# Kernel optimization log

Hardware: AMD Instinct MI355X
Metric: run time of the kernel (lower is better)

## Reference

```python
import jax, jax.numpy as jnp
import numpy as np

N_NODES = 100000


def sage_conv(x, src, dst, w_self, w_neigh, b):
    # DGL SAGEConv('mean'): h = x @ W_self + mean_{u in N(v)} x_u @ W_neigh + b
    ones = jnp.ones(src.shape[0], dtype=x.dtype)
    deg = jax.ops.segment_sum(ones, dst, num_segments=N_NODES)  # [N]
    neigh_sum = jax.ops.segment_sum(x[src], dst, num_segments=N_NODES)  # [N, F]
    neigh = neigh_sum / jnp.clip(deg, 1.0)[:, None]  # isolated nodes -> 0
    return x @ w_self + neigh @ w_neigh + b


def setup_inputs() -> dict:
    key = jax.random.key(0)
    ks = jax.random.split(key, 9)
    nfeat, nhid, nclass = 128, 128, 2
    E = 1600000
    x = jax.random.normal(ks[0], (N_NODES, nfeat), dtype=jnp.float32)
    src = jax.random.randint(ks[1], (E,), 0, N_NODES)
    dst = jax.random.randint(ks[2], (E,), 0, N_NODES)
    s1 = 1.0 / np.sqrt(nfeat)
    s2 = 1.0 / np.sqrt(nhid)
    return {
        "x": x,
        "src": src,
        "dst": dst,
        "w_self1": jax.random.uniform(ks[3], (nfeat, nhid), jnp.float32, -s1, s1),
        "w_neigh1": jax.random.uniform(ks[4], (nfeat, nhid), jnp.float32, -s1, s1),
        "b1": jnp.zeros((nhid,), jnp.float32),
        "w_self2": jax.random.uniform(ks[5], (nhid, nclass), jnp.float32, -s2, s2),
        "w_neigh2": jax.random.uniform(ks[6], (nhid, nclass), jnp.float32, -s2, s2),
        "b2": jnp.zeros((nclass,), jnp.float32),
    }


def reference(x, src, dst, w_self1, w_neigh1, b1, w_self2, w_neigh2, b2):
    h = jax.nn.relu(sage_conv(x, src, dst, w_self1, w_neigh1, b1))
    h = sage_conv(h, src, dst, w_self2, w_neigh2, b2)
    return jax.nn.log_softmax(h, axis=1)
```

## Files before the change

kernel.cpp:

```cpp
#include <hip/hip_runtime.h>
#include <hip/hip_bf16.h>


#define N_FEAT 128
#define CSHIFT 10
#define CNODES 1024
#define CCAP 18432
#define BATCH 4096

typedef __attribute__((ext_vector_type(8))) short short8;
typedef __attribute__((ext_vector_type(8))) unsigned short ushort8_t;
typedef __attribute__((ext_vector_type(16))) float f32x16;

__global__ __launch_bounds__(256) void multisplit_kernel(
    const int* __restrict__ src, const int* __restrict__ dst,
    int* __restrict__ ccursor, unsigned* __restrict__ cbuf, int E) {
    __shared__ unsigned stage[BATCH];
    __shared__ int cnt[128];
    __shared__ int s[128];
    __shared__ int excl[128];
    __shared__ int incl[128];
    __shared__ int cur[128];
    __shared__ int gpos[128];
    int tid = threadIdx.x;
    int base = blockIdx.x * BATCH;
    int total = min(BATCH, E - base);

    unsigned pk[16];
    int bn[16];
    if (tid < 128) cnt[tid] = 0;
    __syncthreads();
    #pragma unroll
    for (int k = 0; k < 16; ++k) {
        int e = base + k * 256 + tid;
        if (e < E) {
            int d = dst[e];
            int sv = src[e];
            bn[k] = d >> CSHIFT;
            pk[k] = ((unsigned)(d & (CNODES - 1)) << 17) | (unsigned)sv;
            atomicAdd(&cnt[bn[k]], 1);
        } else {
            bn[k] = -1;
        }
    }
    __syncthreads();
    int c = (tid < 128) ? cnt[tid] : 0;
    int val = c;
    if (tid < 128) s[tid] = val;
    __syncthreads();
    for (int off = 1; off < 128; off <<= 1) {
        int t = (tid >= off && tid < 128) ? s[tid - off] : 0;
        __syncthreads();
        if (tid < 128) { val += t; s[tid] = val; }
        __syncthreads();
    }
    if (tid < 128) {
        incl[tid] = val;
        excl[tid] = val - c;
        cur[tid] = val - c;
        gpos[tid] = (c > 0) ? atomicAdd(&ccursor[tid], c) : 0;
    }
    __syncthreads();
    #pragma unroll
    for (int k = 0; k < 16; ++k) {
        if (bn[k] >= 0) {
            int ofs = atomicAdd(&cur[bn[k]], 1);
            stage[ofs] = pk[k];
        }
    }
    __syncthreads();
    for (int i = tid; i < total; i += 256) {
        int lo = 0, hi = 127;
        while (lo < hi) {
            int mid = (lo + hi) >> 1;
            if (incl[mid] > i) hi = mid; else lo = mid + 1;
        }
        int b = lo;
        int target = gpos[b] + (i - excl[b]);
        cbuf[(size_t)b * CCAP + target] = stage[i];
    }
}

__global__ void coarse_scan_kernel(const int* __restrict__ ccnt, int* __restrict__ cstart,
                                   int* __restrict__ row_ptr, int nbk, int N, int E) {
    __shared__ int s[128];
    int tid = threadIdx.x;
    int c = (tid < nbk) ? ccnt[tid] : 0;
    int val = c;
    s[tid] = val;
    __syncthreads();
    for (int off = 1; off < 128; off <<= 1) {
        int t = (tid >= off) ? s[tid - off] : 0;
        __syncthreads();
        val += t;
        s[tid] = val;
        __syncthreads();
    }
    if (tid < nbk) cstart[tid] = val - c;
    if (tid == 0) row_ptr[N] = E;
}

__global__ __launch_bounds__(1024) void build_csr2_kernel(
    const unsigned* __restrict__ cbuf, const int* __restrict__ ccnt,
    const int* __restrict__ cstart, int* __restrict__ row_ptr,
    int* __restrict__ csr, int N) {
    __shared__ int hist[CNODES];
    __shared__ int s[CNODES];
    __shared__ int cur[CNODES];
    int cb = blockIdx.x;
    int tid = threadIdx.x;
    int cnt = ccnt[cb];
    int base = cstart[cb];
    size_t bbase = (size_t)cb * CCAP;
    hist[tid] = 0;
    __syncthreads();
    for (int e = tid; e < cnt; e += 1024) {
        unsigned p = cbuf[bbase + e];
        atomicAdd(&hist[p >> 17], 1);
    }
    __syncthreads();
    int c = hist[tid];
    int val = c;
    s[tid] = val;
    __syncthreads();
    for (int off = 1; off < 1024; off <<= 1) {
        int t = (tid >= off) ? s[tid - off] : 0;
        __syncthreads();
        val += t;
        s[tid] = val;
        __syncthreads();
    }
    int excl = val - c;
    int node = cb * CNODES + tid;
    if (node < N) row_ptr[node] = base + excl;
    cur[tid] = excl;
    __syncthreads();
    for (int e = tid; e < cnt; e += 1024) {
        unsigned p = cbuf[bbase + e];
        int bin = p >> 17;
        int ofs = atomicAdd(&cur[bin], 1);
        csr[base + ofs] = (int)(p & 0x1FFFF);
    }
}

__global__ void to_bf16_kernel(const float* __restrict__ x, ushort* __restrict__ xb, int n4) {
    int i = blockIdx.x * 256 + threadIdx.x;
    int stride = gridDim.x * 256;
    for (; i < n4; i += stride) {
        float4 v = ((const float4*)x)[i];
        ushort4 r;
        r.x = __bfloat16_as_ushort(__float2bfloat16(v.x));
        r.y = __bfloat16_as_ushort(__float2bfloat16(v.y));
        r.z = __bfloat16_as_ushort(__float2bfloat16(v.z));
        r.w = __bfloat16_as_ushort(__float2bfloat16(v.w));
        ((ushort4*)xb)[i] = r;
    }
}

__global__ void prep_weights_kernel(const float* __restrict__ w1, const float* __restrict__ w2,
                                    ushort* __restrict__ wt) {
    int id = blockIdx.x * 256 + threadIdx.x;
    if (id >= 128 * 256) return;
    int nn = id >> 8;
    int k = id & 255;
    float v = (k < 128) ? w1[k * 128 + nn] : w2[(k - 128) * 128 + nn];
    wt[nn * 256 + k] = __bfloat16_as_ushort(__float2bfloat16(v));
}

__device__ __forceinline__ float bf16_bits_to_f32(ushort u) {
    union { unsigned int i; float f; } c;
    c.i = ((unsigned int)u) << 16;
    return c.f;
}

__global__ void aggregate_bf16_kernel(const ushort* __restrict__ xb,
                                      const int* __restrict__ row_ptr,
                                      const int* __restrict__ csr,
                                      ushort* __restrict__ out, int n) {
    int v = blockIdx.x * 4 + (threadIdx.x >> 6);
    int lane = threadIdx.x & 63;
    if (v >= n) return;
    int beg = row_ptr[v];
    int end = row_ptr[v + 1];
    float a0 = 0.f, b0 = 0.f, a1 = 0.f, b1 = 0.f;
    int e = beg;
    for (; e + 4 <= end; e += 4) {
        int s0 = csr[e], s1 = csr[e + 1], s2 = csr[e + 2], s3 = csr[e + 3];
        ushort2 t0 = ((const ushort2*)(xb + (size_t)s0 * N_FEAT))[lane];
        ushort2 t1 = ((const ushort2*)(xb + (size_t)s1 * N_FEAT))[lane];
        ushort2 t2 = ((const ushort2*)(xb + (size_t)s2 * N_FEAT))[lane];
        ushort2 t3 = ((const ushort2*)(xb + (size_t)s3 * N_FEAT))[lane];
        a0 += bf16_bits_to_f32(t0.x); b0 += bf16_bits_to_f32(t0.y);
        a1 += bf16_bits_to_f32(t1.x); b1 += bf16_bits_to_f32(t1.y);
        a0 += bf16_bits_to_f32(t2.x); b0 += bf16_bits_to_f32(t2.y);
        a1 += bf16_bits_to_f32(t3.x); b1 += bf16_bits_to_f32(t3.y);
    }
    for (; e < end; ++e) {
        int s0 = csr[e];
        ushort2 t0 = ((const ushort2*)(xb + (size_t)s0 * N_FEAT))[lane];
        a0 += bf16_bits_to_f32(t0.x); b0 += bf16_bits_to_f32(t0.y);
    }
    int deg = end - beg;
    float inv = (deg > 0) ? 1.0f / (float)deg : 0.0f;
    ushort2 r;
    r.x = __bfloat16_as_ushort(__float2bfloat16((a0 + a1) * inv));
    r.y = __bfloat16_as_ushort(__float2bfloat16((b0 + b1) * inv));
    ((ushort2*)(out + (size_t)v * N_FEAT))[lane] = r;
}

__global__ __launch_bounds__(256) void gemm1_mfma_kernel(
    const ushort* __restrict__ xb, const ushort* __restrict__ nbb,
    const ushort* __restrict__ wt, const float* __restrict__ b,
    ushort* __restrict__ h, int n) {
    __shared__ ushort As[128 * 72];
    __shared__ ushort Bs[128 * 72];
    int tid = threadIdx.x;
    int wave = tid >> 6;
    int lane = tid & 63;
    int m = lane & 31;
    int half = lane >> 5;
    int block_row = blockIdx.x * 128;

    f32x16 acc[4];
    #pragma unroll
    for (int t = 0; t < 4; ++t)
        #pragma unroll
        for (int i = 0; i < 16; ++i) acc[t][i] = 0.0f;

    for (int kc = 0; kc < 4; ++kc) {
        const ushort* A = (kc < 2) ? xb : nbb;
        int k0 = (kc & 1) * 64;
        #pragma unroll
        for (int l = 0; l < 4; ++l) {
            int idx = l * 256 + tid;
            int r = idx >> 3;
            int p = idx & 7;
            int node = block_row + r;
            ushort8_t v;
            if (node < n) {
                v = *(const ushort8_t*)(A + (size_t)node * N_FEAT + k0 + p * 8);
            } else {
                #pragma unroll
                for (int q = 0; q < 8; ++q) v[q] = 0;
            }
            *(ushort8_t*)(&As[r * 72 + p * 8]) = v;
        }
        #pragma unroll
        for (int l = 0; l < 4; ++l) {
            int idx = l * 256 + tid;
            int cc = idx >> 3;
            int p = idx & 7;
            ushort8_t v = *(const ushort8_t*)(wt + (size_t)cc * 256 + kc * 64 + p * 8);
            *(ushort8_t*)(&Bs[cc * 72 + p * 8]) = v;
        }
        __syncthreads();
        #pragma unroll
        for (int ks = 0; ks < 4; ++ks) {
            int koff = ks * 16 + half * 8;
            short8 a = *(const short8*)(&As[(32 * wave + m) * 72 + koff]);
            short8 bf0 = *(const short8*)(&Bs[(0 * 32 + m) * 72 + koff]);
            short8 bf1 = *(const short8*)(&Bs[(1 * 32 + m) * 72 + koff]);
            short8 bf2 = *(const short8*)(&Bs[(2 * 32 + m) * 72 + koff]);
            short8 bf3 = *(const short8*)(&Bs[(3 * 32 + m) * 72 + koff]);
            acc[0] = __builtin_amdgcn_mfma_f32_32x32x16_bf16(a, bf0, acc[0], 0, 0, 0);
            acc[1] = __builtin_amdgcn_mfma_f32_32x32x16_bf16(a, bf1, acc[1], 0, 0, 0);
            acc[2] = __builtin_amdgcn_mfma_f32_32x32x16_bf16(a, bf2, acc[2], 0, 0, 0);
            acc[3] = __builtin_amdgcn_mfma_f32_32x32x16_bf16(a, bf3, acc[3], 0, 0, 0);
        }
        __syncthreads();
    }
    #pragma unroll
    for (int t = 0; t < 4; ++t) {
        int col = t * 32 + m;
        float bias = b[col];
        #pragma unroll
        for (int reg = 0; reg < 16; ++reg) {
            int rowin = (reg & 3) + 8 * (reg >> 2) + 4 * half;
            int node = block_row + 32 * wave + rowin;
            if (node < n) {
                float v = fmaxf(acc[t][reg] + bias, 0.0f);
                h[(size_t)node * N_FEAT + col] = __bfloat16_as_ushort(__float2bfloat16(v));
            }
        }
    }
}

__global__ void layer2a_kernel(const ushort* __restrict__ h,
                               const float* __restrict__ ws, const float* __restrict__ wn,
                               float* __restrict__ s_out, float* __restrict__ z_out, int n) {
    int v = blockIdx.x * 4 + (threadIdx.x >> 6);
    int lane = threadIdx.x & 63;
    if (v >= n) return;
    ushort2 hb = ((const ushort2*)(h + (size_t)v * N_FEAT))[lane];
    float hx = bf16_bits_to_f32(hb.x);
    float hy = bf16_bits_to_f32(hb.y);
    float4 w0 = ((const float4*)ws)[lane];
    float4 w1 = ((const float4*)wn)[lane];
    float p0 = hx * w0.x + hy * w0.z;
    float p1 = hx * w0.y + hy * w0.w;
    float q0 = hx * w1.x + hy * w1.z;
    float q1 = hx * w1.y + hy * w1.w;
    #pragma unroll
    for (int off = 32; off > 0; off >>= 1) {
        p0 += __shfl_xor(p0, off);
        p1 += __shfl_xor(p1, off);
        q0 += __shfl_xor(q0, off);
        q1 += __shfl_xor(q1, off);
    }
    if (lane == 0) {
        ((float2*)s_out)[v] = make_float2(p0, p1);
        ((float2*)z_out)[v] = make_float2(q0, q1);
    }
}

__global__ void layer2b_kernel(const float* __restrict__ s_in, const float* __restrict__ z,
                               const int* __restrict__ row_ptr, const int* __restrict__ csr,
                               const float* __restrict__ b, float* __restrict__ out, int n) {
    int v = blockIdx.x * 256 + threadIdx.x;
    if (v >= n) return;
    int beg = row_ptr[v];
    int end = row_ptr[v + 1];
    float a0 = 0.f, a1 = 0.f, c0 = 0.f, c1 = 0.f;
    int e = beg;
    for (; e + 2 <= end; e += 2) {
        float2 t0 = ((const float2*)z)[csr[e]];
        float2 t1 = ((const float2*)z)[csr[e + 1]];
        a0 += t0.x; a1 += t0.y;
        c0 += t1.x; c1 += t1.y;
    }
    if (e < end) {
        float2 t0 = ((const float2*)z)[csr[e]];
        a0 += t0.x; a1 += t0.y;
    }
    int deg = end - beg;
    float inv = (deg > 0) ? 1.0f / (float)deg : 0.0f;
    float2 sv = ((const float2*)s_in)[v];
    float o0 = sv.x + (a0 + c0) * inv + b[0];
    float o1 = sv.y + (a1 + c1) * inv + b[1];
    float mx = fmaxf(o0, o1);
    float lse = mx + logf(expf(o0 - mx) + expf(o1 - mx));
    ((float2*)out)[v] = make_float2(o0 - lse, o1 - lse);
}

extern "C" void kernel_launch(void* const* d_in, const int* in_sizes, int n_in,
                              void* d_out, int out_size, void* d_ws, size_t ws_size,
                              hipStream_t stream) {
    const float* x        = (const float*)d_in[0];
    const int*   src      = (const int*)d_in[1];
    const int*   dst      = (const int*)d_in[2];
    const float* w_self1  = (const float*)d_in[3];
    const float* w_neigh1 = (const float*)d_in[4];
    const float* b1       = (const float*)d_in[5];
    const float* w_self2  = (const float*)d_in[6];
    const float* w_neigh2 = (const float*)d_in[7];
    const float* b2       = (const float*)d_in[8];
    float* out = (float*)d_out;

    int N = in_sizes[0] / N_FEAT;
    int E = in_sizes[1];
    int nbk = (N + CNODES - 1) / CNODES;

    char* ws = (char*)d_ws;
    size_t off = 0;
    auto alloc = [&](size_t bytes) -> void* {
        void* p = ws + off;
        off += (bytes + 255) & ~(size_t)255;
        return p;
    };
    int*      ccursor = (int*)alloc(128 * 4);
    int*      cstart  = (int*)alloc(128 * 4);
    int*      row_ptr = (int*)alloc((size_t)(N + 1) * 4);
    int*      csr     = (int*)alloc((size_t)E * 4);
    unsigned* cbuf    = (unsigned*)alloc((size_t)nbk * CCAP * 4);
    ushort*   xb      = (ushort*)alloc((size_t)N * N_FEAT * 2);
    ushort*   nbb     = (ushort*)alloc((size_t)N * N_FEAT * 2);
    ushort*   h       = (ushort*)alloc((size_t)N * N_FEAT * 2);
    ushort*   wt      = (ushort*)alloc((size_t)128 * 256 * 2);
    float*    s_buf   = (float*)alloc((size_t)N * 2 * 4);
    float*    z_buf   = (float*)alloc((size_t)N * 2 * 4);
    (void)ws_size; (void)n_in; (void)out_size;

    hipMemsetAsync(ccursor, 0, 128 * 4, stream);

    multisplit_kernel<<<(E + BATCH - 1) / BATCH, 256, 0, stream>>>(src, dst, ccursor, cbuf, E);
    coarse_scan_kernel<<<1, 128, 0, stream>>>(ccursor, cstart, row_ptr, nbk, N, E);
    build_csr2_kernel<<<nbk, 1024, 0, stream>>>(cbuf, ccursor, cstart, row_ptr, csr, N);

    to_bf16_kernel<<<1024, 256, 0, stream>>>(x, xb, N * N_FEAT / 4);
    prep_weights_kernel<<<(128 * 256 + 255) / 256, 256, 0, stream>>>(w_self1, w_neigh1, wt);
    aggregate_bf16_kernel<<<(N + 3) / 4, 256, 0, stream>>>(xb, row_ptr, csr, nbb, N);
    gemm1_mfma_kernel<<<(N + 127) / 128, 256, 0, stream>>>(xb, nbb, wt, b1, h, N);
    layer2a_kernel<<<(N + 3) / 4, 256, 0, stream>>>(h, w_self2, w_neigh2, s_buf, z_buf, N);
    layer2b_kernel<<<(N + 255) / 256, 256, 0, stream>>>(s_buf, z_buf, row_ptr, csr, b2, out, N);
}
```

Baseline: 284.2 us.

## Fuse preprocessing kernels, inline coarse scan, fuse layer-2 projection into GEMM epilogue

Merges the edge multisplit, bf16 conversion of x and weight packing into one launch with role-split blocks. The coarse scan moves into each build_csr2 block, and multisplit uses per-wave counters to cut LDS atomic contention. The aggregation loop is unrolled to 8 edges, and the layer-2 projection is fused into the GEMM1 epilogue, which removes the h buffer round trip and two launches. Costs are redundant scans per block and extra shuffle reductions in the GEMM epilogue.

```diff
diff --git a/kernel.cpp b/kernel.cpp
--- a/kernel.cpp
+++ b/kernel.cpp
@@ -7,28 +7,60 @@
 #define CNODES 1024
 #define CCAP 18432
 #define BATCH 4096
+#define BF_BLOCKS 256
+#define PW_BLOCKS 128
 
 typedef __attribute__((ext_vector_type(8))) short short8;
 typedef __attribute__((ext_vector_type(8))) unsigned short ushort8_t;
 typedef __attribute__((ext_vector_type(16))) float f32x16;
 
-__global__ __launch_bounds__(256) void multisplit_kernel(
+__global__ __launch_bounds__(256) void prep_and_split_kernel(
     const int* __restrict__ src, const int* __restrict__ dst,
-    int* __restrict__ ccursor, unsigned* __restrict__ cbuf, int E) {
+    int* __restrict__ ccursor, unsigned* __restrict__ cbuf, int E,
+    const float* __restrict__ x, ushort* __restrict__ xb, int n4,
+    const float* __restrict__ w1, const float* __restrict__ w2,
+    ushort* __restrict__ wt, int nms) {
     __shared__ unsigned stage[BATCH];
-    __shared__ int cnt[128];
+    __shared__ int cntw[4][128];
+    __shared__ int curw[4][128];
     __shared__ int s[128];
     __shared__ int excl[128];
     __shared__ int incl[128];
-    __shared__ int cur[128];
     __shared__ int gpos[128];
     int tid = threadIdx.x;
-    int base = blockIdx.x * BATCH;
+    int bid = blockIdx.x;
+
+    if (bid >= nms) {
+        int rb = bid - nms;
+        if (rb < BF_BLOCKS) {
+            int i = rb * 256 + tid;
+            int stride = BF_BLOCKS * 256;
+            for (; i < n4; i += stride) {
+                float4 v = ((const float4*)x)[i];
+                ushort4 r;
+                r.x = __bfloat16_as_ushort(__float2bfloat16(v.x));
+                r.y = __bfloat16_as_ushort(__float2bfloat16(v.y));
+                r.z = __bfloat16_as_ushort(__float2bfloat16(v.z));
+                r.w = __bfloat16_as_ushort(__float2bfloat16(v.w));
+                ((ushort4*)xb)[i] = r;
+            }
+        } else {
+            int id = (rb - BF_BLOCKS) * 256 + tid;
+            int nn = id >> 8;
+            int k = id & 255;
+            float v = (k < 128) ? w1[k * 128 + nn] : w2[(k - 128) * 128 + nn];
+            wt[nn * 256 + k] = __bfloat16_as_ushort(__float2bfloat16(v));
+        }
+        return;
+    }
+
+    int wv = tid >> 6;
+    int base = bid * BATCH;
     int total = min(BATCH, E - base);
 
     unsigned pk[16];
     int bn[16];
-    if (tid < 128) cnt[tid] = 0;
+    for (int i = tid; i < 512; i += 256) ((int*)cntw)[i] = 0;
     __syncthreads();
     #pragma unroll
     for (int k = 0; k < 16; ++k) {
@@ -38,16 +70,24 @@
             int sv = src[e];
             bn[k] = d >> CSHIFT;
             pk[k] = ((unsigned)(d & (CNODES - 1)) << 17) | (unsigned)sv;
-            atomicAdd(&cnt[bn[k]], 1);
+            atomicAdd(&cntw[wv][bn[k]], 1);
         } else {
             bn[k] = -1;
         }
     }
     __syncthreads();
-    int c = (tid < 128) ? cnt[tid] : 0;
+    int c = 0;
+    if (tid < 128) {
+        int c0 = cntw[0][tid], c1 = cntw[1][tid], c2 = cntw[2][tid], c3 = cntw[3][tid];
+        cntw[0][tid] = 0;
+        cntw[1][tid] = c0;
+        cntw[2][tid] = c0 + c1;
+        cntw[3][tid] = c0 + c1 + c2;
+        c = c0 + c1 + c2 + c3;
+        s[tid] = c;
+    }
+    __syncthreads();
     int val = c;
-    if (tid < 128) s[tid] = val;
-    __syncthreads();
     for (int off = 1; off < 128; off <<= 1) {
         int t = (tid >= off && tid < 128) ? s[tid - off] : 0;
         __syncthreads();
@@ -56,15 +96,19 @@
     }
     if (tid < 128) {
         incl[tid] = val;
-        excl[tid] = val - c;
-        cur[tid] = val - c;
+        int e0 = val - c;
+        excl[tid] = e0;
+        curw[0][tid] = e0 + cntw[0][tid];
+        curw[1][tid] = e0 + cntw[1][tid];
+        curw[2][tid] = e0 + cntw[2][tid];
+        curw[3][tid] = e0 + cntw[3][tid];
         gpos[tid] = (c > 0) ? atomicAdd(&ccursor[tid], c) : 0;
     }
     __syncthreads();
     #pragma unroll
     for (int k = 0; k < 16; ++k) {
         if (bn[k] >= 0) {
-            int ofs = atomicAdd(&cur[bn[k]], 1);
+            int ofs = atomicAdd(&curw[wv][bn[k]], 1);
             stage[ofs] = pk[k];
         }
     }
@@ -81,37 +125,33 @@
     }
 }
 
-__global__ void coarse_scan_kernel(const int* __restrict__ ccnt, int* __restrict__ cstart,
-                                   int* __restrict__ row_ptr, int nbk, int N, int E) {
-    __shared__ int s[128];
-    int tid = threadIdx.x;
-    int c = (tid < nbk) ? ccnt[tid] : 0;
-    int val = c;
-    s[tid] = val;
-    __syncthreads();
-    for (int off = 1; off < 128; off <<= 1) {
-        int t = (tid >= off) ? s[tid - off] : 0;
-        __syncthreads();
-        val += t;
-        s[tid] = val;
-        __syncthreads();
-    }
-    if (tid < nbk) cstart[tid] = val - c;
-    if (tid == 0) row_ptr[N] = E;
-}
-
 __global__ __launch_bounds__(1024) void build_csr2_kernel(
     const unsigned* __restrict__ cbuf, const int* __restrict__ ccnt,
-    const int* __restrict__ cstart, int* __restrict__ row_ptr,
-    int* __restrict__ csr, int N) {
+    int* __restrict__ row_ptr, int* __restrict__ csr, int N, int E) {
     __shared__ int hist[CNODES];
     __shared__ int s[CNODES];
     __shared__ int cur[CNODES];
+    __shared__ int cstart_s;
     int cb = blockIdx.x;
     int tid = threadIdx.x;
+
+    int c0 = 0;
+    if (tid < 128) { c0 = ccnt[tid]; s[tid] = c0; }
+    __syncthreads();
+    int v128 = c0;
+    for (int off = 1; off < 128; off <<= 1) {
+        int t = (tid >= off && tid < 128) ? s[tid - off] : 0;
+        __syncthreads();
+        if (tid < 128) { v128 += t; s[tid] = v128; }
+        __syncthreads();
+    }
+    if (tid == cb) cstart_s = v128 - c0;
+    if (cb == 0 && tid == 0) row_ptr[N] = E;
+    __syncthreads();
     int cnt = ccnt[cb];
-    int base = cstart[cb];
+    int base = cstart_s;
     size_t bbase = (size_t)cb * CCAP;
+
     hist[tid] = 0;
     __syncthreads();
     for (int e = tid; e < cnt; e += 1024) {
@@ -141,30 +181,6 @@
         int ofs = atomicAdd(&cur[bin], 1);
         csr[base + ofs] = (int)(p & 0x1FFFF);
     }
-}
-
-__global__ void to_bf16_kernel(const float* __restrict__ x, ushort* __restrict__ xb, int n4) {
-    int i = blockIdx.x * 256 + threadIdx.x;
-    int stride = gridDim.x * 256;
-    for (; i < n4; i += stride) {
-        float4 v = ((const float4*)x)[i];
-        ushort4 r;
-        r.x = __bfloat16_as_ushort(__float2bfloat16(v.x));
-        r.y = __bfloat16_as_ushort(__float2bfloat16(v.y));
-        r.z = __bfloat16_as_ushort(__float2bfloat16(v.z));
-        r.w = __bfloat16_as_ushort(__float2bfloat16(v.w));
-        ((ushort4*)xb)[i] = r;
-    }
-}
-
-__global__ void prep_weights_kernel(const float* __restrict__ w1, const float* __restrict__ w2,
-                                    ushort* __restrict__ wt) {
-    int id = blockIdx.x * 256 + threadIdx.x;
-    if (id >= 128 * 256) return;
-    int nn = id >> 8;
-    int k = id & 255;
-    float v = (k < 128) ? w1[k * 128 + nn] : w2[(k - 128) * 128 + nn];
-    wt[nn * 256 + k] = __bfloat16_as_ushort(__float2bfloat16(v));
 }
 
 __device__ __forceinline__ float bf16_bits_to_f32(ushort u) {
@@ -184,6 +200,26 @@
     int end = row_ptr[v + 1];
     float a0 = 0.f, b0 = 0.f, a1 = 0.f, b1 = 0.f;
     int e = beg;
+    for (; e + 8 <= end; e += 8) {
+        int s0 = csr[e],     s1 = csr[e + 1], s2 = csr[e + 2], s3 = csr[e + 3];
+        int s4 = csr[e + 4], s5 = csr[e + 5], s6 = csr[e + 6], s7 = csr[e + 7];
+        ushort2 t0 = ((const ushort2*)(xb + (size_t)s0 * N_FEAT))[lane];
+        ushort2 t1 = ((const ushort2*)(xb + (size_t)s1 * N_FEAT))[lane];
+        ushort2 t2 = ((const ushort2*)(xb + (size_t)s2 * N_FEAT))[lane];
+        ushort2 t3 = ((const ushort2*)(xb + (size_t)s3 * N_FEAT))[lane];
+        ushort2 t4 = ((const ushort2*)(xb + (size_t)s4 * N_FEAT))[lane];
+        ushort2 t5 = ((const ushort2*)(xb + (size_t)s5 * N_FEAT))[lane];
+        ushort2 t6 = ((const ushort2*)(xb + (size_t)s6 * N_FEAT))[lane];
+        ushort2 t7 = ((const ushort2*)(xb + (size_t)s7 * N_FEAT))[lane];
+        a0 += bf16_bits_to_f32(t0.x); b0 += bf16_bits_to_f32(t0.y);
+        a1 += bf16_bits_to_f32(t1.x); b1 += bf16_bits_to_f32(t1.y);
+        a0 += bf16_bits_to_f32(t2.x); b0 += bf16_bits_to_f32(t2.y);
+        a1 += bf16_bits_to_f32(t3.x); b1 += bf16_bits_to_f32(t3.y);
+        a0 += bf16_bits_to_f32(t4.x); b0 += bf16_bits_to_f32(t4.y);
+        a1 += bf16_bits_to_f32(t5.x); b1 += bf16_bits_to_f32(t5.y);
+        a0 += bf16_bits_to_f32(t6.x); b0 += bf16_bits_to_f32(t6.y);
+        a1 += bf16_bits_to_f32(t7.x); b1 += bf16_bits_to_f32(t7.y);
+    }
     for (; e + 4 <= end; e += 4) {
         int s0 = csr[e], s1 = csr[e + 1], s2 = csr[e + 2], s3 = csr[e + 3];
         ushort2 t0 = ((const ushort2*)(xb + (size_t)s0 * N_FEAT))[lane];
@@ -208,10 +244,11 @@
     ((ushort2*)(out + (size_t)v * N_FEAT))[lane] = r;
 }
 
-__global__ __launch_bounds__(256) void gemm1_mfma_kernel(
+__global__ __launch_bounds__(256) void gemm1_fused_kernel(
     const ushort* __restrict__ xb, const ushort* __restrict__ nbb,
     const ushort* __restrict__ wt, const float* __restrict__ b,
-    ushort* __restrict__ h, int n) {
+    const float* __restrict__ ws2, const float* __restrict__ wn2,
+    float* __restrict__ s_out, float* __restrict__ z_out, int n) {
     __shared__ ushort As[128 * 72];
     __shared__ ushort Bs[128 * 72];
     int tid = threadIdx.x;
@@ -269,47 +306,39 @@
         }
         __syncthreads();
     }
+
+    float bcol[4], wsc[4][2], wnc[4][2];
     #pragma unroll
     for (int t = 0; t < 4; ++t) {
         int col = t * 32 + m;
-        float bias = b[col];
-        #pragma unroll
-        for (int reg = 0; reg < 16; ++reg) {
-            int rowin = (reg & 3) + 8 * (reg >> 2) + 4 * half;
-            int node = block_row + 32 * wave + rowin;
-            if (node < n) {
-                float v = fmaxf(acc[t][reg] + bias, 0.0f);
-                h[(size_t)node * N_FEAT + col] = __bfloat16_as_ushort(__float2bfloat16(v));
-            }
-        }
-    }
-}
-
-__global__ void layer2a_kernel(const ushort* __restrict__ h,
-                               const float* __restrict__ ws, const float* __restrict__ wn,
-                               float* __restrict__ s_out, float* __restrict__ z_out, int n) {
-    int v = blockIdx.x * 4 + (threadIdx.x >> 6);
-    int lane = threadIdx.x & 63;
-    if (v >= n) return;
-    ushort2 hb = ((const ushort2*)(h + (size_t)v * N_FEAT))[lane];
-    float hx = bf16_bits_to_f32(hb.x);
-    float hy = bf16_bits_to_f32(hb.y);
-    float4 w0 = ((const float4*)ws)[lane];
-    float4 w1 = ((const float4*)wn)[lane];
-    float p0 = hx * w0.x + hy * w0.z;
-    float p1 = hx * w0.y + hy * w0.w;
-    float q0 = hx * w1.x + hy * w1.z;
-    float q1 = hx * w1.y + hy * w1.w;
+        bcol[t] = b[col];
+        float2 a = ((const float2*)ws2)[col];
+        float2 q = ((const float2*)wn2)[col];
+        wsc[t][0] = a.x; wsc[t][1] = a.y;
+        wnc[t][0] = q.x; wnc[t][1] = q.y;
+    }
     #pragma unroll
-    for (int off = 32; off > 0; off >>= 1) {
-        p0 += __shfl_xor(p0, off);
-        p1 += __shfl_xor(p1, off);
-        q0 += __shfl_xor(q0, off);
-        q1 += __shfl_xor(q1, off);
-    }
-    if (lane == 0) {
-        ((float2*)s_out)[v] = make_float2(p0, p1);
-        ((float2*)z_out)[v] = make_float2(q0, q1);
+    for (int reg = 0; reg < 16; ++reg) {
+        int rowin = (reg & 3) + 8 * (reg >> 2) + 4 * half;
+        int node = block_row + 32 * wave + rowin;
+        float p0 = 0.f, p1 = 0.f, q0 = 0.f, q1 = 0.f;
+        #pragma unroll
+        for (int t = 0; t < 4; ++t) {
+            float hv = fmaxf(acc[t][reg] + bcol[t], 0.0f);
+            p0 += hv * wsc[t][0]; p1 += hv * wsc[t][1];
+            q0 += hv * wnc[t][0]; q1 += hv * wnc[t][1];
+        }
+        #pragma unroll
+        for (int off = 1; off < 32; off <<= 1) {
+            p0 += __shfl_xor(p0, off);
+            p1 += __shfl_xor(p1, off);
+            q0 += __shfl_xor(q0, off);
+            q1 += __shfl_xor(q1, off);
+        }
+        if (m == 0 && node < n) {
+            ((float2*)s_out)[node] = make_float2(p0, p1);
+            ((float2*)z_out)[node] = make_float2(q0, q1);
+        }
     }
 }
 
@@ -359,6 +388,7 @@
     int N = in_sizes[0] / N_FEAT;
     int E = in_sizes[1];
     int nbk = (N + CNODES - 1) / CNODES;
+    int nms = (E + BATCH - 1) / BATCH;
 
     char* ws = (char*)d_ws;
     size_t off = 0;
@@ -368,13 +398,11 @@
         return p;
     };
     int*      ccursor = (int*)alloc(128 * 4);
-    int*      cstart  = (int*)alloc(128 * 4);
     int*      row_ptr = (int*)alloc((size_t)(N + 1) * 4);
     int*      csr     = (int*)alloc((size_t)E * 4);
     unsigned* cbuf    = (unsigned*)alloc((size_t)nbk * CCAP * 4);
     ushort*   xb      = (ushort*)alloc((size_t)N * N_FEAT * 2);
     ushort*   nbb     = (ushort*)alloc((size_t)N * N_FEAT * 2);
-    ushort*   h       = (ushort*)alloc((size_t)N * N_FEAT * 2);
     ushort*   wt      = (ushort*)alloc((size_t)128 * 256 * 2);
     float*    s_buf   = (float*)alloc((size_t)N * 2 * 4);
     float*    z_buf   = (float*)alloc((size_t)N * 2 * 4);
@@ -382,14 +410,11 @@
 
     hipMemsetAsync(ccursor, 0, 128 * 4, stream);
 
-    multisplit_kernel<<<(E + BATCH - 1) / BATCH, 256, 0, stream>>>(src, dst, ccursor, cbuf, E);
-    coarse_scan_kernel<<<1, 128, 0, stream>>>(ccursor, cstart, row_ptr, nbk, N, E);
-    build_csr2_kernel<<<nbk, 1024, 0, stream>>>(cbuf, ccursor, cstart, row_ptr, csr, N);
-
-    to_bf16_kernel<<<1024, 256, 0, stream>>>(x, xb, N * N_FEAT / 4);
-    prep_weights_kernel<<<(128 * 256 + 255) / 256, 256, 0, stream>>>(w_self1, w_neigh1, wt);
+    prep_and_split_kernel<<<nms + BF_BLOCKS + PW_BLOCKS, 256, 0, stream>>>(
+        src, dst, ccursor, cbuf, E, x, xb, N * N_FEAT / 4, w_self1, w_neigh1, wt, nms);
+    build_csr2_kernel<<<nbk, 1024, 0, stream>>>(cbuf, ccursor, row_ptr, csr, N, E);
     aggregate_bf16_kernel<<<(N + 3) / 4, 256, 0, stream>>>(xb, row_ptr, csr, nbb, N);
-    gemm1_mfma_kernel<<<(N + 127) / 128, 256, 0, stream>>>(xb, nbb, wt, b1, h, N);
-    layer2a_kernel<<<(N + 3) / 4, 256, 0, stream>>>(h, w_self2, w_neigh2, s_buf, z_buf, N);
+    gemm1_fused_kernel<<<(N + 127) / 128, 256, 0, stream>>>(
+        xb, nbb, wt, b1, w_self2, w_neigh2, s_buf, z_buf, N);
     layer2b_kernel<<<(N + 255) / 256, 256, 0, stream>>>(s_buf, z_buf, row_ptr, csr, b2, out, N);
 }
```

New measurement: 250.3 us. -11.9%, faster.
